# Performance work log

Measured on AMD Instinct MI355X. Metric: run time of the kernel, lower is better.

Reference implementation:

```python
import jax, jax.numpy as jnp
import numpy as np
import math

B, S, D = 2, 2048, 768
H, KS, VS = 12, 64, 64
MAX_DIST, NUM_BASES, MIN_HALF_LIFE = 1000, 16, 3.0


def _exponential_basis_features():
    # positions -max_dist..max_dist, exponential basis as in RelativePositionalBias
    positions = np.arange(-MAX_DIST, MAX_DIST + 1)
    abs_pos = np.abs(positions).astype(np.float32)
    max_range = math.log2(MAX_DIST)
    half_lives = np.power(2.0, np.linspace(MIN_HALF_LIFE, max_range, NUM_BASES)).reshape(1, -1)
    feats = np.exp(-math.log(2.0) * abs_pos[:, None] / half_lives)  # [2*max_dist+1, num_bases]
    return jnp.asarray(feats, dtype=jnp.float32)


def setup_inputs() -> dict:
    key = jax.random.key(0)
    ks = jax.random.split(key, 6)
    x = jax.random.normal(ks[0], (B, S, D), dtype=jnp.float32)
    # torch nn.Linear weight convention: [out_features, in_features], applied as x @ W.T
    Wq = jax.random.normal(ks[1], (H * KS, D), dtype=jnp.float32) * 0.02
    Wk = jax.random.normal(ks[2], (H * KS, D), dtype=jnp.float32) * 0.02
    Wv = jax.random.normal(ks[3], (H * VS, D), dtype=jnp.float32) * 0.02
    # original zero-inits w_o; use small random for a non-degenerate correctness baseline
    Wo = jax.random.normal(ks[4], (D, H * VS), dtype=jnp.float32) * 0.02
    basis_weights = jax.random.normal(ks[5], (H, NUM_BASES), dtype=jnp.float32)
    basis_features = _exponential_basis_features()  # buffer (non-learned)
    return {"x": x, "Wq": Wq, "Wk": Wk, "Wv": Wv, "Wo": Wo,
            "basis_weights": basis_weights, "basis_features": basis_features}


def _relative_bias(basis_features, basis_weights, q_len, k_len):
    rel = jnp.arange(k_len)[None, :] - jnp.arange(q_len)[:, None]
    rel = jnp.clip(rel, -MAX_DIST, MAX_DIST) + MAX_DIST  # [q, k] indices
    basis = basis_features[rel]                          # [q, k, nb]
    return jnp.einsum('qkb,hb->hqk', basis, basis_weights)


def reference(x, Wq, Wk, Wv, Wo, basis_weights, basis_features):
    b, s, _ = x.shape
    q = (x @ Wq.T).reshape(b, s, H, KS)
    k = (x @ Wk.T).reshape(b, s, H, KS)
    v = (x @ Wv.T).reshape(b, s, H, VS)
    scale = math.sqrt(KS)
    scores = jnp.einsum('bqhc,bkhc->bhqk', q, k) / scale
    scores = scores + _relative_bias(basis_features, basis_weights, s, s)[None]
    attn = jax.nn.softmax(scores, axis=-1)  # dropout is identity in eval
    out = jnp.einsum('bhqk,bkhv->bqhv', attn, v).reshape(b, s, H * VS)
    out = out @ Wo.T
    return out, attn
```

## Files before the change

kernel.cpp:

```cpp
#include <hip/hip_runtime.h>

typedef _Float16 f16;
typedef __attribute__((ext_vector_type(4))) _Float16 f16x4;
typedef __attribute__((ext_vector_type(8))) _Float16 f16x8;
typedef __attribute__((ext_vector_type(4))) float f32x4;
typedef __attribute__((ext_vector_type(16))) float f32x16;

#define B_ 2
#define S_ 2048
#define DMODEL 768
#define H_ 12
#define HS 64
#define NB_ 16
#define QKV_LD 2304

#define ZERO16 {0.f,0.f,0.f,0.f,0.f,0.f,0.f,0.f,0.f,0.f,0.f,0.f,0.f,0.f,0.f,0.f}

__device__ __forceinline__ void gload16(const f16* g, f16* lds) {
    __builtin_amdgcn_global_load_lds((const __attribute__((address_space(1))) void*)g,
                                     (__attribute__((address_space(3))) void*)lds, 16, 0, 0);
}
#define WAIT_VM0_BARRIER()  do { asm volatile("s_waitcnt vmcnt(0)" ::: "memory"); \
                                 __builtin_amdgcn_s_barrier(); } while (0)

__global__ __launch_bounds__(256) void prep_kernel(const float* __restrict__ x,
                                                   const float* __restrict__ Wq,
                                                   const float* __restrict__ Wk,
                                                   const float* __restrict__ Wv,
                                                   const float* __restrict__ Wo,
                                                   const float* __restrict__ bw,
                                                   const float* __restrict__ bf,
                                                   f16* __restrict__ xb,
                                                   f16* __restrict__ wqkv16,
                                                   f16* __restrict__ wo16,
                                                   float* __restrict__ biasTab) {
    int bid = blockIdx.x;
    int t = threadIdx.x;
    if (bid < 5376) {
        const float* src;
        f16* dst;
        float scale = 1.0f;
        int i;
        if (bid < 3072) {
            i = bid * 256 + t; src = x; dst = xb;
        } else if (bid < 4800) {
            i = (bid - 3072) * 256 + t;
            dst = wqkv16;
            if (i < 147456)      { src = Wq; scale = 0.18033688011112f; }
            else if (i < 294912) { src = Wk - 147456 * 4; }
            else                 { src = Wv - 294912 * 4; }
        } else {
            i = (bid - 4800) * 256 + t; src = Wo; dst = wo16;
        }
        f32x4 v = reinterpret_cast<const f32x4*>(src)[i];
        union { f16 h[4]; unsigned long long u; } o;
        o.h[0] = (f16)(v.x * scale);
        o.h[1] = (f16)(v.y * scale);
        o.h[2] = (f16)(v.z * scale);
        o.h[3] = (f16)(v.w * scale);
        reinterpret_cast<unsigned long long*>(dst)[i] = o.u;
    } else {
        int idx = (bid - 5376) * 256 + t;
        if (idx >= H_ * 4095) return;
        int h = idx / 4095, d = idx % 4095;
        int rel = min(1000, max(-1000, d - 2047));
        int r = rel + 1000;
        float s = 0.f;
#pragma unroll
        for (int tt = 0; tt < NB_; ++tt) s += bf[r * NB_ + tt] * bw[h * NB_ + tt];
        biasTab[h * 4095 + d] = s * 1.44269504088896f;
    }
}

__global__ __launch_bounds__(256) void vtrans_kernel(const f16* __restrict__ qkv,
                                                     f16* __restrict__ vt) {
    __shared__ f16 tile[64][72];
    int blk = blockIdx.x;
    int tb = blk & 31;
    int bh = blk >> 5;
    int b = bh / H_;
    int tok0 = tb << 6;
    int t = threadIdx.x;
    const f16* src = qkv + (size_t)b * S_ * QKV_LD + 1536 + (bh - b * H_) * 64;
#pragma unroll
    for (int j = 0; j < 2; ++j) {
        int u = t + (j << 8);
        int r = u >> 3, c = (u & 7) << 3;
        *reinterpret_cast<f16x8*>(&tile[r][c]) =
            *reinterpret_cast<const f16x8*>(src + (size_t)(tok0 + r) * QKV_LD + c);
    }
    __syncthreads();
    f16* dst = vt + (size_t)bh * 64 * S_ + tok0;
#pragma unroll
    for (int j = 0; j < 2; ++j) {
        int u = t + (j << 8);
        int v = u >> 3, tc = (u & 7) << 3;
        union { f16 h8[8]; f16x8 v8; } o;
#pragma unroll
        for (int i = 0; i < 8; ++i) o.h8[i] = tile[tc + i][v];
        *reinterpret_cast<f16x8*>(&dst[(size_t)v * S_ + tc]) = o.v8;
    }
}

template <typename OutT>
__global__ __launch_bounds__(256) void gemm_nt(const f16* __restrict__ A,
                                               const f16* __restrict__ Bm,
                                               OutT* __restrict__ C,
                                               int M, int N, int K, float alpha) {
    __shared__ __align__(16) f16 As[2][128 * 32];
    __shared__ __align__(16) f16 Bs[2][128 * 32];
    const int tiles_n = N >> 7;
    int tm = blockIdx.x / tiles_n, tn = blockIdx.x % tiles_n;
    int m0 = tm << 7, n0 = tn << 7;
    int t = threadIdx.x;
    int w = t >> 6, l = t & 63;
    int wr = w >> 1, wc = w & 1;
    int fr = l & 15, hi = l >> 4;
    f32x4 acc[4][4] = {};

#define GEMM_STAGE(buf, k0)                                                        \
    do {                                                                           \
        _Pragma("unroll")                                                          \
        for (int j = 0; j < 2; ++j) {                                              \
            int u = t + (j << 8);                                                  \
            int row = u >> 2, ch = u & 3;                                          \
            int gcol = (k0) + ((ch ^ (row & 3)) << 3);                             \
            gload16(&A[(size_t)(m0 + row) * K + gcol], As[buf] + (w << 9) + (j << 11)); \
            gload16(&Bm[(size_t)(n0 + row) * K + gcol], Bs[buf] + (w << 9) + (j << 11)); \
        }                                                                          \
    } while (0)

    const int nk = K >> 5;
    GEMM_STAGE(0, 0);
    WAIT_VM0_BARRIER();
    for (int kt = 0; kt < nk; ++kt) {
        int buf = kt & 1;
        if (kt + 1 < nk) GEMM_STAGE(buf ^ 1, (kt + 1) << 5);
        f16x8 af[4], bfv[4];
#pragma unroll
        for (int m = 0; m < 4; ++m) {
            int row = wr * 64 + m * 16 + fr;
            af[m] = *reinterpret_cast<const f16x8*>(&As[buf][row * 32 + ((hi ^ (fr & 3)) << 3)]);
        }
#pragma unroll
        for (int n = 0; n < 4; ++n) {
            int row = wc * 64 + n * 16 + fr;
            bfv[n] = *reinterpret_cast<const f16x8*>(&Bs[buf][row * 32 + ((hi ^ (fr & 3)) << 3)]);
        }
#pragma unroll
        for (int m = 0; m < 4; ++m)
#pragma unroll
            for (int n = 0; n < 4; ++n)
                acc[m][n] = __builtin_amdgcn_mfma_f32_16x16x32_f16(af[m], bfv[n], acc[m][n], 0, 0, 0);
        WAIT_VM0_BARRIER();
    }
#undef GEMM_STAGE
    int cc = l & 15, cr = (l >> 4) << 2;
#pragma unroll
    for (int m = 0; m < 4; ++m)
#pragma unroll
        for (int n = 0; n < 4; ++n)
#pragma unroll
            for (int j = 0; j < 4; ++j) {
                int rg = m0 + wr * 64 + m * 16 + cr + j;
                int cg = n0 + wc * 64 + n * 16 + cc;
                C[(size_t)rg * N + cg] = (OutT)(acc[m][n][j] * alpha);
            }
}

#define PSWZ(row) ((((row) >> 2) & 3) << 3)
__global__ __launch_bounds__(256, 3) void attn_kernel(const f16* __restrict__ qp,
                                                      const f16* __restrict__ kp,
                                                      const f16* __restrict__ vt,
                                                      const float* __restrict__ biasTab,
                                                      float* __restrict__ attn_out,
                                                      f16* __restrict__ ctx_out) {
    __shared__ __align__(16) union {
        f16 ks1[2][128 * 64];
        struct { f16 ks[2][64 * 64]; f16 vs[2][64 * 64]; } p2;
    } ar;
    __shared__ __align__(16) f16 psh[64][72];
    __shared__ float bias_l[2112];
    __shared__ float red_l[64][2];
    __shared__ float li_s[64];

    int orig = blockIdx.x;
    int blk = (orig & 7) * 96 + (orig >> 3);
    int qt = blk & 31;
    int bh = blk >> 5;
    int h = bh % H_;
    int b = bh / H_;
    int q0 = qt << 6;

    int t = threadIdx.x;
    int w = t >> 6, l = t & 63;
    int wq = w >> 1, wk = w & 1;
    int col = l & 31;
    int hi = l >> 5;
    int hi4 = hi << 2, hi8 = hi << 3;

    const size_t rowbase = (size_t)b * S_ * QKV_LD + (size_t)h * HS;
    const f16* vbase = vt + (size_t)bh * HS * S_;

    f16x8 qf[4];
    {
        const f16* qrow = qp + rowbase + (size_t)(q0 + wq * 32 + col) * QKV_LD + hi8;
#pragma unroll
        for (int ci = 0; ci < 4; ++ci) qf[ci] = *reinterpret_cast<const f16x8*>(qrow + ci * 16);
    }

    {
        const float* bt = biasTab + h * 4095 + (1984 - q0);
        for (int i = t; i < 2111; i += 256) bias_l[i] = bt[i];
    }

#define P1_STAGE(buf, kb0)                                                          \
    do {                                                                            \
        _Pragma("unroll")                                                           \
        for (int j = 0; j < 4; ++j) {                                               \
            int u = t + (j << 8);                                                   \
            int row = u >> 3, ch = u & 7;                                           \
            gload16(kp + rowbase + (size_t)((kb0) + row) * QKV_LD + ((ch ^ (row & 7)) << 3), \
                    ar.ks1[buf] + (w << 9) + (j << 11));                            \
        }                                                                           \
    } while (0)

    float lsum[16];
#pragma unroll
    for (int r = 0; r < 16; ++r) lsum[r] = 0.f;

    P1_STAGE(0, 0);
    WAIT_VM0_BARRIER();
    for (int jt = 0; jt < 16; ++jt) {
        int buf = jt & 1;
        if (jt + 1 < 16) P1_STAGE(buf ^ 1, (jt + 1) << 7);
#pragma unroll
        for (int half = 0; half < 2; ++half) {
            int krow = half * 64 + wk * 32 + col;
            f32x16 s = ZERO16;
#pragma unroll
            for (int ci = 0; ci < 4; ++ci) {
                f16x8 kf = *reinterpret_cast<const f16x8*>(
                    &ar.ks1[buf][krow * 64 + (((ci * 2 + hi) ^ (krow & 7)) << 3)]);
                s = __builtin_amdgcn_mfma_f32_32x32x16_f16(qf[ci], kf, s, 0, 0, 0);
            }
            int kcol = (jt << 7) + krow;
            const float* bl = bias_l + (kcol + 63 - (wq * 32 + hi4));
#pragma unroll
            for (int r = 0; r < 16; ++r) {
                const int cr = (r & 3) + 8 * (r >> 2);
                lsum[r] += __builtin_amdgcn_exp2f(s[r] + bl[-cr]);
            }
        }
        WAIT_VM0_BARRIER();
    }
#undef P1_STAGE

#pragma unroll
    for (int off = 1; off < 32; off <<= 1) {
#pragma unroll
        for (int r = 0; r < 16; ++r) lsum[r] += __shfl_xor(lsum[r], off);
    }
    if (col == 0) {
#pragma unroll
        for (int r = 0; r < 16; ++r)
            red_l[wq * 32 + (r & 3) + 8 * (r >> 2) + hi4][wk] = lsum[r];
    }
    __syncthreads();
    if (t < 64) li_s[t] = 1.0f / (red_l[t][0] + red_l[t][1]);
    __syncthreads();
    float lreg[16];
#pragma unroll
    for (int r = 0; r < 16; ++r) lreg[r] = li_s[wq * 32 + (r & 3) + 8 * (r >> 2) + hi4];

#define P2_STAGE(buf, kb0)                                                          \
    do {                                                                            \
        _Pragma("unroll")                                                           \
        for (int j = 0; j < 2; ++j) {                                               \
            int u = t + (j << 8);                                                   \
            int row = u >> 3, ch = u & 7;                                           \
            int sw = ((ch ^ (row & 7)) << 3);                                       \
            gload16(kp + rowbase + (size_t)((kb0) + row) * QKV_LD + sw,             \
                    ar.p2.ks[buf] + (w << 9) + (j << 11));                          \
            gload16(vbase + (size_t)row * S_ + (kb0) + sw,                          \
                    ar.p2.vs[buf] + (w << 9) + (j << 11));                          \
        }                                                                           \
    } while (0)

    f32x16 oacc = ZERO16;
    float* aout = attn_out + (((size_t)b * H_ + h) * S_ + q0) * S_;
    const int kcol_loc = wk * 32 + col;

    P2_STAGE(0, 0);
    WAIT_VM0_BARRIER();
    for (int tix = 0; tix < 32; ++tix) {
        int buf = tix & 1;
        int kb0 = tix << 6;
        if (tix + 1 < 32) P2_STAGE(buf ^ 1, kb0 + 64);
        f32x16 s = ZERO16;
#pragma unroll
        for (int ci = 0; ci < 4; ++ci) {
            f16x8 kf = *reinterpret_cast<const f16x8*>(
                &ar.p2.ks[buf][kcol_loc * 64 + (((ci * 2 + hi) ^ (kcol_loc & 7)) << 3)]);
            s = __builtin_amdgcn_mfma_f32_32x32x16_f16(qf[ci], kf, s, 0, 0, 0);
        }
        int kcol = kb0 + kcol_loc;
        const float* bl = bias_l + (kcol + 63 - (wq * 32 + hi4));
#pragma unroll
        for (int r = 0; r < 16; ++r) {
            const int cr = (r & 3) + 8 * (r >> 2);
            int row = wq * 32 + cr + hi4;
            float p = __builtin_amdgcn_exp2f(s[r] + bl[-cr]) * lreg[r];
            __builtin_nontemporal_store(p, &aout[(size_t)row * S_ + kcol]);
            psh[row][kcol_loc ^ PSWZ(row)] = (f16)p;
        }
        asm volatile("s_waitcnt lgkmcnt(0)" ::: "memory");
        __builtin_amdgcn_s_barrier();
        __builtin_amdgcn_sched_barrier(0);
        {
            const int rowq = wq * 32 + col;
            const int sw = PSWZ(rowq);
#pragma unroll
            for (int ci = 0; ci < 4; ++ci) {
                f16x8 pa = *reinterpret_cast<const f16x8*>(&psh[rowq][(ci * 16 + hi8) ^ sw]);
                f16x8 vf = *reinterpret_cast<const f16x8*>(
                    &ar.p2.vs[buf][kcol_loc * 64 + (((ci * 2 + hi) ^ (kcol_loc & 7)) << 3)]);
                oacc = __builtin_amdgcn_mfma_f32_32x32x16_f16(pa, vf, oacc, 0, 0, 0);
            }
        }
        __syncthreads();
    }
#undef P2_STAGE

    {
        f16* cbase = ctx_out + ((size_t)b * S_ + q0) * DMODEL + h * HS + kcol_loc;
#pragma unroll
        for (int r = 0; r < 16; ++r) {
            int row = wq * 32 + (r & 3) + 8 * (r >> 2) + hi4;
            cbase[(size_t)row * DMODEL] = (f16)oacc[r];
        }
    }
}

extern "C" void kernel_launch(void* const* d_in, const int* in_sizes, int n_in,
                              void* d_out, int out_size, void* d_ws, size_t ws_size,
                              hipStream_t stream) {
    const float* x     = (const float*)d_in[0];
    const float* Wq    = (const float*)d_in[1];
    const float* Wk    = (const float*)d_in[2];
    const float* Wv    = (const float*)d_in[3];
    const float* Wo    = (const float*)d_in[4];
    const float* bw    = (const float*)d_in[5];
    const float* bfeat = (const float*)d_in[6];

    char* ws = (char*)d_ws;
    f16*   xb      = (f16*)(ws + 0);
    f16*   vt      = (f16*)(ws + 0);
    f16*   qkv     = (f16*)(ws + 6291456);
    f16*   ctx     = (f16*)(ws + 25165824);
    f16*   wqkv16  = (f16*)(ws + 31457280);
    f16*   wo16    = (f16*)(ws + 34996224);
    float* biasTab = (float*)(ws + 36175872);

    float* out0 = (float*)d_out;
    float* attn = out0 + (size_t)B_ * S_ * DMODEL;

    prep_kernel<<<5568, 256, 0, stream>>>(x, Wq, Wk, Wv, Wo, bw, bfeat,
                                          xb, wqkv16, wo16, biasTab);

    gemm_nt<f16><<<32 * 18, 256, 0, stream>>>(xb, wqkv16, qkv, 4096, QKV_LD, 768, 1.0f);

    vtrans_kernel<<<768, 256, 0, stream>>>(qkv, vt);

    attn_kernel<<<B_ * H_ * (S_ / 64), 256, 0, stream>>>(
        qkv + 0, qkv + 768, vt, biasTab, attn, ctx);

    gemm_nt<float><<<32 * 6, 256, 0, stream>>>(ctx, wo16, out0, 4096, DMODEL, 768, 1.0f);
}
```

Measured before the change: 173.8 us.

## Defer attention-probability stores past the PV MFMA and narrow output GEMM tiles

In the attention kernel, the fp32 probability values are held in registers and their nontemporal global stores are issued after the PV MFMAs and the end-of-iteration barrier. This lets the large attention-matrix write stream overlap the next tile's compute, where before it sat in front of the LDS barrier. The end-of-loop __syncthreads is replaced by an explicit vmcnt wait plus s_barrier, and the wait macro now also waits on lgkmcnt. Separately, the GEMM is templated on its N tile width, and the output projection uses 64-wide tiles so it launches 384 blocks instead of 192 for better CU occupancy. The cost is 16 extra registers in the attention kernel and a changed wait structure.

```diff
diff --git a/kernel.cpp b/kernel.cpp
--- a/kernel.cpp
+++ b/kernel.cpp
@@ -20,7 +20,7 @@
     __builtin_amdgcn_global_load_lds((const __attribute__((address_space(1))) void*)g,
                                      (__attribute__((address_space(3))) void*)lds, 16, 0, 0);
 }
-#define WAIT_VM0_BARRIER()  do { asm volatile("s_waitcnt vmcnt(0)" ::: "memory"); \
+#define WAIT_VM0_BARRIER()  do { asm volatile("s_waitcnt vmcnt(0) lgkmcnt(0)" ::: "memory"); \
                                  __builtin_amdgcn_s_barrier(); } while (0)
 
 __global__ __launch_bounds__(256) void prep_kernel(const float* __restrict__ x,
@@ -102,21 +102,23 @@
     }
 }
 
-template <typename OutT>
+template <typename OutT, int NT>
 __global__ __launch_bounds__(256) void gemm_nt(const f16* __restrict__ A,
                                                const f16* __restrict__ Bm,
                                                OutT* __restrict__ C,
                                                int M, int N, int K, float alpha) {
+    constexpr int NF  = NT / 32;
+    constexpr int BCH = NT / 64;
     __shared__ __align__(16) f16 As[2][128 * 32];
-    __shared__ __align__(16) f16 Bs[2][128 * 32];
-    const int tiles_n = N >> 7;
+    __shared__ __align__(16) f16 Bs[2][NT * 32];
+    const int tiles_n = N / NT;
     int tm = blockIdx.x / tiles_n, tn = blockIdx.x % tiles_n;
-    int m0 = tm << 7, n0 = tn << 7;
+    int m0 = tm << 7, n0 = tn * NT;
     int t = threadIdx.x;
     int w = t >> 6, l = t & 63;
     int wr = w >> 1, wc = w & 1;
     int fr = l & 15, hi = l >> 4;
-    f32x4 acc[4][4] = {};
+    f32x4 acc[4][NF] = {};
 
 #define GEMM_STAGE(buf, k0)                                                        \
     do {                                                                           \
@@ -126,6 +128,12 @@
             int row = u >> 2, ch = u & 3;                                          \
             int gcol = (k0) + ((ch ^ (row & 3)) << 3);                             \
             gload16(&A[(size_t)(m0 + row) * K + gcol], As[buf] + (w << 9) + (j << 11)); \
+        }                                                                          \
+        _Pragma("unroll")                                                          \
+        for (int j = 0; j < BCH; ++j) {                                            \
+            int u = t + (j << 8);                                                  \
+            int row = u >> 2, ch = u & 3;                                          \
+            int gcol = (k0) + ((ch ^ (row & 3)) << 3);                             \
             gload16(&Bm[(size_t)(n0 + row) * K + gcol], Bs[buf] + (w << 9) + (j << 11)); \
         }                                                                          \
     } while (0)
@@ -136,21 +144,21 @@
     for (int kt = 0; kt < nk; ++kt) {
         int buf = kt & 1;
         if (kt + 1 < nk) GEMM_STAGE(buf ^ 1, (kt + 1) << 5);
-        f16x8 af[4], bfv[4];
+        f16x8 af[4], bfv[NF];
 #pragma unroll
         for (int m = 0; m < 4; ++m) {
             int row = wr * 64 + m * 16 + fr;
             af[m] = *reinterpret_cast<const f16x8*>(&As[buf][row * 32 + ((hi ^ (fr & 3)) << 3)]);
         }
 #pragma unroll
-        for (int n = 0; n < 4; ++n) {
-            int row = wc * 64 + n * 16 + fr;
+        for (int n = 0; n < NF; ++n) {
+            int row = wc * (NT / 2) + n * 16 + fr;
             bfv[n] = *reinterpret_cast<const f16x8*>(&Bs[buf][row * 32 + ((hi ^ (fr & 3)) << 3)]);
         }
 #pragma unroll
         for (int m = 0; m < 4; ++m)
 #pragma unroll
-            for (int n = 0; n < 4; ++n)
+            for (int n = 0; n < NF; ++n)
                 acc[m][n] = __builtin_amdgcn_mfma_f32_16x16x32_f16(af[m], bfv[n], acc[m][n], 0, 0, 0);
         WAIT_VM0_BARRIER();
     }
@@ -159,11 +167,11 @@
 #pragma unroll
     for (int m = 0; m < 4; ++m)
 #pragma unroll
-        for (int n = 0; n < 4; ++n)
+        for (int n = 0; n < NF; ++n)
 #pragma unroll
             for (int j = 0; j < 4; ++j) {
                 int rg = m0 + wr * 64 + m * 16 + cr + j;
-                int cg = n0 + wc * 64 + n * 16 + cc;
+                int cg = n0 + wc * (NT / 2) + n * 16 + cc;
                 C[(size_t)rg * N + cg] = (OutT)(acc[m][n][j] * alpha);
             }
 }
@@ -293,10 +301,12 @@
 
     P2_STAGE(0, 0);
     WAIT_VM0_BARRIER();
+    float pstash[16];
     for (int tix = 0; tix < 32; ++tix) {
         int buf = tix & 1;
         int kb0 = tix << 6;
         if (tix + 1 < 32) P2_STAGE(buf ^ 1, kb0 + 64);
+        __builtin_amdgcn_sched_barrier(0);
         f32x16 s = ZERO16;
 #pragma unroll
         for (int ci = 0; ci < 4; ++ci) {
@@ -311,7 +321,7 @@
             const int cr = (r & 3) + 8 * (r >> 2);
             int row = wq * 32 + cr + hi4;
             float p = __builtin_amdgcn_exp2f(s[r] + bl[-cr]) * lreg[r];
-            __builtin_nontemporal_store(p, &aout[(size_t)row * S_ + kcol]);
+            pstash[r] = p;
             psh[row][kcol_loc ^ PSWZ(row)] = (f16)p;
         }
         asm volatile("s_waitcnt lgkmcnt(0)" ::: "memory");
@@ -328,7 +338,14 @@
                 oacc = __builtin_amdgcn_mfma_f32_32x32x16_f16(pa, vf, oacc, 0, 0, 0);
             }
         }
-        __syncthreads();
+        asm volatile("s_waitcnt vmcnt(0)" ::: "memory");
+        __builtin_amdgcn_s_barrier();
+#pragma unroll
+        for (int r = 0; r < 16; ++r) {
+            const int cr = (r & 3) + 8 * (r >> 2);
+            int row = wq * 32 + cr + hi4;
+            __builtin_nontemporal_store(pstash[r], &aout[(size_t)row * S_ + kcol]);
+        }
     }
 #undef P2_STAGE
 
@@ -368,12 +385,12 @@
     prep_kernel<<<5568, 256, 0, stream>>>(x, Wq, Wk, Wv, Wo, bw, bfeat,
                                           xb, wqkv16, wo16, biasTab);
 
-    gemm_nt<f16><<<32 * 18, 256, 0, stream>>>(xb, wqkv16, qkv, 4096, QKV_LD, 768, 1.0f);
+    gemm_nt<f16, 128><<<32 * 18, 256, 0, stream>>>(xb, wqkv16, qkv, 4096, QKV_LD, 768, 1.0f);
 
     vtrans_kernel<<<768, 256, 0, stream>>>(qkv, vt);
 
     attn_kernel<<<B_ * H_ * (S_ / 64), 256, 0, stream>>>(
         qkv + 0, qkv + 768, vt, biasTab, attn, ctx);
 
-    gemm_nt<float><<<32 * 6, 256, 0, stream>>>(ctx, wo16, out0, 4096, DMODEL, 768, 1.0f);
-}
+    gemm_nt<float, 64><<<32 * 12, 256, 0, stream>>>(ctx, wo16, out0, 4096, DMODEL, 768, 1.0f);
+}
```

Measured after the change: 171.8 us (median of 2 runs). About the same (-1.2%).
